# Kernel tuning notes

Measured on AMD Instinct MI355X. Metric: run time of the kernel, lower is better.

## Reference

```python
import jax, jax.numpy as jnp
import numpy as np

H, B, N, F, O = 8, 2, 2048, 256, 64
NEG_INF = jnp.float32(-9e15)


def _xavier(key, shape):
    fan_in, fan_out = shape[-2], shape[-1]
    limit = np.sqrt(6.0 / (fan_in + fan_out))
    return jax.random.uniform(key, shape, dtype=jnp.float32, minval=-limit, maxval=limit)


def setup_inputs() -> dict:
    key = jax.random.key(0)
    k1, k2, k3, k4, k5 = jax.random.split(key, 5)
    x = jax.random.normal(k1, (B, N, F), dtype=jnp.float32)
    adj = (jax.random.uniform(k2, (B, N, N)) < 0.05).astype(jnp.float32)
    adj = jnp.maximum(adj, jnp.eye(N, dtype=jnp.float32))
    W = _xavier(k3, (H, F, O))           # self.linear
    a_src = _xavier(k4, (H, O, 1))       # attention_vect_src
    a_dst = _xavier(k5, (H, O, 1))       # attention_vect_dst
    return {"x": x, "adj": adj, "W": W, "a_src": a_src, "a_dst": a_dst}


def reference(x, adj, W, a_src, a_dst):
    # h: [H, B, N, O]  (per-head linear projection)
    h = jnp.einsum('bnf,hfo->hbno', x, W)
    # additive attention scalars per node: [H, B, N]
    s_src = jnp.einsum('hbno,ho->hbn', h, a_src[..., 0])
    s_dst = jnp.einsum('hbno,ho->hbn', h, a_dst[..., 0])
    # score[h,b,i,j] = s_dst[i] + s_src[j]  -> [H, B, N, N]
    score = s_dst[..., :, None] + s_src[..., None, :]
    score = jax.nn.leaky_relu(score, negative_slope=0.2)
    score = jnp.where(adj > 0, score, NEG_INF)
    att = jax.nn.softmax(score, axis=-1) * adj  # dropout = identity (eval)
    # weighted aggregation of neighbor features: [H, B, N, O]
    out = jnp.einsum('hbij,hbjo->hbio', att, h)
    # concat heads along feature dim (head order preserved): [B, N, H*O]
    out = jnp.transpose(out, (1, 2, 0, 3)).reshape(B, N, H * O)
    return jax.nn.relu(out)
```

## Files before the change

### kernel.cpp

```cpp
#include <hip/hip_runtime.h>

#define H_ 8
#define B_ 2
#define N_ 2048
#define F_ 256
#define O_ 64
#define CAP 256

typedef unsigned short u16;
typedef unsigned int   u32;
typedef __attribute__((ext_vector_type(8))) short bf16x8;
typedef __attribute__((ext_vector_type(4))) float f32x4;

__device__ __forceinline__ float us2f(u16 u) {
    union { u32 i; float f; } c; c.i = ((u32)u) << 16; return c.f;
}
__device__ __forceinline__ float hi2f(u32 w) {
    union { u32 i; float f; } c; c.i = w & 0xFFFF0000u; return c.f;
}
__device__ __forceinline__ float lo2f(u32 w) {
    union { u32 i; float f; } c; c.i = w << 16; return c.f;
}
__device__ __forceinline__ u16 f2us_rn(float f) {
    union { float f; u32 i; } c; c.f = f;
    u32 r = c.i + 0x7FFFu + ((c.i >> 16) & 1u);
    return (u16)(r >> 16);
}
__device__ __forceinline__ int detect_bf(const void* adj) {
    u32 w0 = *(const u32*)adj;
    return (w0 & 0xFFFFu) == 0x3F80u;
}

__global__ __launch_bounds__(256) void wt_kernel(const void* __restrict__ W,
                                                 const void* __restrict__ adj,
                                                 u16* __restrict__ Wt) {
    int bf = detect_bf(adj);
    int g  = blockIdx.x * 256 + threadIdx.x;
    int h  = g >> 11;
    int o  = (g >> 5) & 63;
    int fc = g & 31;
    u16 tmp[8];
    if (bf) {
        const u16* wg = (const u16*)W + (size_t)h * F_ * O_ + o;
#pragma unroll
        for (int q = 0; q < 8; ++q) tmp[q] = wg[(size_t)(fc * 8 + q) * O_];
    } else {
        const float* wg = (const float*)W + (size_t)h * F_ * O_ + o;
#pragma unroll
        for (int q = 0; q < 8; ++q) tmp[q] = f2us_rn(wg[(size_t)(fc * 8 + q) * O_]);
    }
    *(uint4*)(Wt + (size_t)h * O_ * F_ + (size_t)o * F_ + fc * 8) = *(uint4*)tmp;
}

__global__ __launch_bounds__(256) void proj_kernel(const void* __restrict__ x,
                                                   const u16* __restrict__ Wt,
                                                   const void* __restrict__ a_src,
                                                   const void* __restrict__ a_dst,
                                                   const void* __restrict__ adj,
                                                   u16* __restrict__ hTb,
                                                   float* __restrict__ sTsrc,
                                                   float* __restrict__ sTdst) {
    int bf   = detect_bf(adj);
    int bx   = blockIdx.x;
    int h    = bx & 7;
    int bn0  = (bx >> 3) * 64;
    int tid  = threadIdx.x;
    int wave = tid >> 6;
    int lane = tid & 63;
    int m_l  = lane & 15;
    int quad = lane >> 4;
    int mrow = bn0 + wave * 16 + m_l;

    const u16* wtb = Wt + (size_t)h * O_ * F_;

    f32x4 acc[4] = {{0,0,0,0},{0,0,0,0},{0,0,0,0},{0,0,0,0}};
#pragma unroll
    for (int ks = 0; ks < 8; ++ks) {
        int kofs = ks * 32 + quad * 8;
        bf16x8 afrag;
        if (bf) {
            afrag = *(const bf16x8*)((const u16*)x + (size_t)mrow * F_ + kofs);
        } else {
            const float* xr = (const float*)x + (size_t)mrow * F_ + kofs;
#pragma unroll
            for (int q = 0; q < 8; ++q) afrag[q] = (short)f2us_rn(xr[q]);
        }
#pragma unroll
        for (int nt = 0; nt < 4; ++nt) {
            bf16x8 bfrag = *(const bf16x8*)(wtb + (size_t)(nt * 16 + m_l) * F_ + kofs);
            acc[nt] = __builtin_amdgcn_mfma_f32_16x16x32_bf16(afrag, bfrag, acc[nt], 0, 0, 0);
        }
    }

    float asv[4], adv[4];
#pragma unroll
    for (int nt = 0; nt < 4; ++nt) {
        int o = nt * 16 + m_l;
        if (bf) {
            asv[nt] = us2f(((const u16*)a_src)[h * 64 + o]);
            adv[nt] = us2f(((const u16*)a_dst)[h * 64 + o]);
        } else {
            asv[nt] = ((const float*)a_src)[h * 64 + o];
            adv[nt] = ((const float*)a_dst)[h * 64 + o];
        }
    }
    float vs[4] = {0,0,0,0}, vd[4] = {0,0,0,0};
#pragma unroll
    for (int nt = 0; nt < 4; ++nt)
#pragma unroll
        for (int r = 0; r < 4; ++r) {
            float hv = acc[nt][r];
            int row = wave * 16 + quad * 4 + r;
            hTb[(size_t)(bn0 + row) * 512 + h * 64 + nt * 16 + m_l] = f2us_rn(hv);
            vs[r] = fmaf(hv, asv[nt], vs[r]);
            vd[r] = fmaf(hv, adv[nt], vd[r]);
        }
#pragma unroll
    for (int r = 0; r < 4; ++r)
#pragma unroll
        for (int off = 1; off < 16; off <<= 1) {
            vs[r] += __shfl_xor(vs[r], off);
            vd[r] += __shfl_xor(vd[r], off);
        }
    if (m_l == 0) {
#pragma unroll
        for (int r = 0; r < 4; ++r) {
            int row = wave * 16 + quad * 4 + r;
            sTsrc[(size_t)(bn0 + row) * H_ + h] = vs[r];
            sTdst[(size_t)(bn0 + row) * H_ + h] = vd[r];
        }
    }
}

__global__ __launch_bounds__(256) void GATLayer_88072599371930_kernel(
        const u16* __restrict__ hTb,
        const float* __restrict__ sTsrc,
        const float* __restrict__ sTdst,
        const void* __restrict__ adj,
        float* __restrict__ out) {
    __shared__ int   scnt;
    __shared__ u16   sj[CAP];
    __shared__ float se[CAP * H_];
    __shared__ float mh[H_];
    __shared__ float rzh[H_];
    __shared__ float sdl[H_];
    __shared__ float sred[8 * 192];

    int bi   = blockIdx.x;
    int tid  = threadIdx.x;
    int base = bi & ~(N_ - 1);
    int bf   = detect_bf(adj);

    if (tid == 0) scnt = 0;
    if (tid < 8) sdl[tid] = sTdst[(size_t)bi * H_ + tid];
    __syncthreads();

    if (bf) {
        const u16* arow = (const u16*)adj + (size_t)bi * N_;
        uint4 v = *(const uint4*)(arow + tid * 8);
        u32 w[4] = {v.x, v.y, v.z, v.w};
        int j0 = tid * 8;
#pragma unroll
        for (int q = 0; q < 4; ++q) {
            if (w[q] & 0xFFFFu) { int p = atomicAdd(&scnt, 1); if (p < CAP) sj[p] = (u16)(j0 + 2 * q); }
            if (w[q] >> 16)     { int p = atomicAdd(&scnt, 1); if (p < CAP) sj[p] = (u16)(j0 + 2 * q + 1); }
        }
    } else {
        const float* arow = (const float*)adj + (size_t)bi * N_;
        for (int j = tid; j < N_; j += 256) {
            if (arow[j] > 0.f) { int p = atomicAdd(&scnt, 1); if (p < CAP) sj[p] = (u16)j; }
        }
    }
    __syncthreads();
    int n = scnt < CAP ? scnt : CAP;

    if (n <= 0) {
        out[(size_t)bi * 512 + tid] = 999.0f;
        out[(size_t)bi * 512 + 256 + tid] = 999.0f;
        return;
    }

    int tot = n * H_;
    for (int idx = tid; idx < tot; idx += 256) {
        int k  = idx >> 3;
        int hh = idx & 7;
        int j  = sj[k];
        float v = sdl[hh] + sTsrc[(size_t)(base + j) * H_ + hh];
        v = v > 0.f ? v : 0.2f * v;
        se[idx] = v;
    }
    __syncthreads();

    if (tid < 64) {
        int hh = tid >> 3, kk = tid & 7;
        float lm = -3.4e38f;
        for (int k = kk; k < n; k += 8) lm = fmaxf(lm, se[k * 8 + hh]);
#pragma unroll
        for (int mm = 1; mm < 8; mm <<= 1) lm = fmaxf(lm, __shfl_xor(lm, mm));
        if (kk == 0) mh[hh] = lm;
    }
    __syncthreads();
    for (int idx = tid; idx < tot; idx += 256) {
        int hh = idx & 7;
        se[idx] = __expf(se[idx] - mh[hh]);
    }
    __syncthreads();
    if (tid < 64) {
        int hh = tid >> 3, kk = tid & 7;
        float ls = 0.f;
        for (int k = kk; k < n; k += 8) ls += se[k * 8 + hh];
#pragma unroll
        for (int mm = 1; mm < 8; mm <<= 1) ls += __shfl_xor(ls, mm);
        if (kk == 0) rzh[hh] = 1.f / ls;
    }
    __syncthreads();

    int wv   = tid >> 6;
    int lane = tid & 63;
    int hh   = lane >> 3;
    int oq8  = lane & 7;
    const u16* hb = hTb + (size_t)base * 512 + hh * 64 + oq8 * 8;

    float a0 = 0.f, a1 = 0.f, a2 = 0.f, a3 = 0.f;
    float a4 = 0.f, a5 = 0.f, a6 = 0.f, a7 = 0.f;
    int k = wv;
    for (; k + 4 < n; k += 8) {
        int   j0 = sj[k], j1 = sj[k + 4];
        float w0 = se[k * 8 + hh], w1 = se[(k + 4) * 8 + hh];
        uint4 v0 = *(const uint4*)(hb + (size_t)j0 * 512);
        uint4 v1 = *(const uint4*)(hb + (size_t)j1 * 512);
        a0 = fmaf(w0, lo2f(v0.x), a0); a1 = fmaf(w0, hi2f(v0.x), a1);
        a2 = fmaf(w0, lo2f(v0.y), a2); a3 = fmaf(w0, hi2f(v0.y), a3);
        a4 = fmaf(w0, lo2f(v0.z), a4); a5 = fmaf(w0, hi2f(v0.z), a5);
        a6 = fmaf(w0, lo2f(v0.w), a6); a7 = fmaf(w0, hi2f(v0.w), a7);
        a0 = fmaf(w1, lo2f(v1.x), a0); a1 = fmaf(w1, hi2f(v1.x), a1);
        a2 = fmaf(w1, lo2f(v1.y), a2); a3 = fmaf(w1, hi2f(v1.y), a3);
        a4 = fmaf(w1, lo2f(v1.z), a4); a5 = fmaf(w1, hi2f(v1.z), a5);
        a6 = fmaf(w1, lo2f(v1.w), a6); a7 = fmaf(w1, hi2f(v1.w), a7);
    }
    for (; k < n; k += 4) {
        int   j = sj[k];
        float w = se[k * 8 + hh];
        uint4 v = *(const uint4*)(hb + (size_t)j * 512);
        a0 = fmaf(w, lo2f(v.x), a0); a1 = fmaf(w, hi2f(v.x), a1);
        a2 = fmaf(w, lo2f(v.y), a2); a3 = fmaf(w, hi2f(v.y), a3);
        a4 = fmaf(w, lo2f(v.z), a4); a5 = fmaf(w, hi2f(v.z), a5);
        a6 = fmaf(w, lo2f(v.w), a6); a7 = fmaf(w, hi2f(v.w), a7);
    }

    if (wv) {
        int p = (wv - 1) * 64 + lane;
        sred[0 * 192 + p] = a0; sred[1 * 192 + p] = a1;
        sred[2 * 192 + p] = a2; sred[3 * 192 + p] = a3;
        sred[4 * 192 + p] = a4; sred[5 * 192 + p] = a5;
        sred[6 * 192 + p] = a6; sred[7 * 192 + p] = a7;
    }
    __syncthreads();
    if (wv == 0) {
        float r[8] = {a0, a1, a2, a3, a4, a5, a6, a7};
        float rz = rzh[hh];
#pragma unroll
        for (int e = 0; e < 8; ++e) {
            float t = r[e] + sred[e * 192 + lane] + sred[e * 192 + 64 + lane]
                           + sred[e * 192 + 128 + lane];
            r[e] = fmaxf(t * rz, 0.f);
        }
        float4 o0; o0.x = r[0]; o0.y = r[1]; o0.z = r[2]; o0.w = r[3];
        float4 o1; o1.x = r[4]; o1.y = r[5]; o1.z = r[6]; o1.w = r[7];
        float* op = out + (size_t)bi * 512 + hh * 64 + oq8 * 8;
        *(float4*)op = o0;
        *(float4*)(op + 4) = o1;
    }
}

extern "C" void kernel_launch(void* const* d_in, const int* in_sizes, int n_in,
                              void* d_out, int out_size, void* d_ws, size_t ws_size,
                              hipStream_t stream) {
    const void *x = 0, *adj = 0, *W = 0, *a_src = 0, *a_dst = 0;
    for (int i = 0; i < n_in; ++i) {
        long sz = in_sizes[i];
        if (sz == (long)B_ * N_ * F_)      x = d_in[i];
        else if (sz == (long)B_ * N_ * N_) adj = d_in[i];
        else if (sz == (long)H_ * F_ * O_) W = d_in[i];
        else if (sz == (long)H_ * O_) { if (!a_src) a_src = d_in[i]; else a_dst = d_in[i]; }
    }
    if (!x)     x     = d_in[0];
    if (!adj)   adj   = d_in[1];
    if (!W)     W     = d_in[2];
    if (!a_src) a_src = d_in[3];
    if (!a_dst) a_dst = d_in[4];

    float* out = (float*)d_out;

    char* ws = (char*)d_ws;
    size_t off = 0;
    u16*   hTb   = (u16*)(ws + off);   off += (size_t)B_ * N_ * H_ * O_ * 2;
    float* sTsrc = (float*)(ws + off); off += (size_t)B_ * N_ * H_ * 4;
    float* sTdst = (float*)(ws + off); off += (size_t)B_ * N_ * H_ * 4;
    u16*   Wt    = (u16*)(ws + off);   off += (size_t)H_ * O_ * F_ * 2;

    wt_kernel<<<dim3(64), dim3(256), 0, stream>>>(W, adj, Wt);
    proj_kernel<<<dim3((N_ * B_ / 64) * H_), dim3(256), 0, stream>>>(
        x, Wt, a_src, a_dst, adj, hTb, sTsrc, sTdst);
    GATLayer_88072599371930_kernel<<<dim3(B_ * N_), dim3(256), 0, stream>>>(
        hTb, sTsrc, sTdst, adj, out);
}
```

Before: 128.5 us.

## Replace sparse gather aggregation with dense bitmask-masked MFMA attention tiles

The per-row sparse gather (atomic neighbor compaction, softmax over compacted list, scalar FMA aggregation) becomes a dense flash-style scheme. A prep kernel packs the adjacency into bitmasks and also does the W transpose. The main kernel processes 16 rows by 2 heads per block, computing masked exp scores into LDS as bf16 and multiplying them against a transposed h layout with MFMA. The softmax max is replaced by an upper bound (leaky_relu of s_dst plus the global max of s_src), which avoids a separate max pass but does dense O(N^2) work on a ~5% sparse matrix and risks underflow or precision loss in the bf16 probabilities.

```diff
diff --git a/kernel.cpp b/kernel.cpp
--- a/kernel.cpp
+++ b/kernel.cpp
@@ -5,7 +5,7 @@
 #define N_ 2048
 #define F_ 256
 #define O_ 64
-#define CAP 256
+#define PPAD 264
 
 typedef unsigned short u16;
 typedef unsigned int   u32;
@@ -15,12 +15,6 @@
 __device__ __forceinline__ float us2f(u16 u) {
     union { u32 i; float f; } c; c.i = ((u32)u) << 16; return c.f;
 }
-__device__ __forceinline__ float hi2f(u32 w) {
-    union { u32 i; float f; } c; c.i = w & 0xFFFF0000u; return c.f;
-}
-__device__ __forceinline__ float lo2f(u32 w) {
-    union { u32 i; float f; } c; c.i = w << 16; return c.f;
-}
 __device__ __forceinline__ u16 f2us_rn(float f) {
     union { float f; u32 i; } c; c.f = f;
     u32 r = c.i + 0x7FFFu + ((c.i >> 16) & 1u);
@@ -31,25 +25,55 @@
     return (w0 & 0xFFFFu) == 0x3F80u;
 }
 
-__global__ __launch_bounds__(256) void wt_kernel(const void* __restrict__ W,
-                                                 const void* __restrict__ adj,
-                                                 u16* __restrict__ Wt) {
-    int bf = detect_bf(adj);
-    int g  = blockIdx.x * 256 + threadIdx.x;
-    int h  = g >> 11;
-    int o  = (g >> 5) & 63;
-    int fc = g & 31;
-    u16 tmp[8];
-    if (bf) {
-        const u16* wg = (const u16*)W + (size_t)h * F_ * O_ + o;
-#pragma unroll
-        for (int q = 0; q < 8; ++q) tmp[q] = wg[(size_t)(fc * 8 + q) * O_];
+__global__ __launch_bounds__(256) void prep_kernel(const void* __restrict__ adj,
+                                                   const void* __restrict__ W,
+                                                   u32* __restrict__ mbg,
+                                                   u16* __restrict__ Wt) {
+    int blk = blockIdx.x;
+    int t   = threadIdx.x;
+    int bf  = detect_bf(adj);
+    if (blk < B_ * N_) {
+        __shared__ unsigned char bytes[256];
+        unsigned m8 = 0;
+        if (bf) {
+            const u16* arow = (const u16*)adj + (size_t)blk * N_;
+            uint4 v = *(const uint4*)(arow + t * 8);
+            u32 w[4] = {v.x, v.y, v.z, v.w};
+#pragma unroll
+            for (int q = 0; q < 4; ++q) {
+                if (w[q] & 0xFFFFu) m8 |= 1u << (2 * q);
+                if (w[q] >> 16)     m8 |= 1u << (2 * q + 1);
+            }
+        } else {
+            const float* arow = (const float*)adj + (size_t)blk * N_;
+#pragma unroll
+            for (int q = 0; q < 8; ++q)
+                if (arow[t * 8 + q] > 0.f) m8 |= 1u << q;
+        }
+        bytes[t] = (unsigned char)m8;
+        __syncthreads();
+        if (t < 64) {
+            u32 w = (u32)bytes[4 * t] | ((u32)bytes[4 * t + 1] << 8)
+                  | ((u32)bytes[4 * t + 2] << 16) | ((u32)bytes[4 * t + 3] << 24);
+            mbg[(size_t)blk * 64 + t] = w;
+        }
     } else {
-        const float* wg = (const float*)W + (size_t)h * F_ * O_ + o;
-#pragma unroll
-        for (int q = 0; q < 8; ++q) tmp[q] = f2us_rn(wg[(size_t)(fc * 8 + q) * O_]);
-    }
-    *(uint4*)(Wt + (size_t)h * O_ * F_ + (size_t)o * F_ + fc * 8) = *(uint4*)tmp;
+        int g  = (blk - B_ * N_) * 256 + t;
+        int h  = g >> 11;
+        int o  = (g >> 5) & 63;
+        int fc = g & 31;
+        u16 tmp[8];
+        if (bf) {
+            const u16* wg = (const u16*)W + (size_t)h * F_ * O_ + o;
+#pragma unroll
+            for (int q = 0; q < 8; ++q) tmp[q] = wg[(size_t)(fc * 8 + q) * O_];
+        } else {
+            const float* wg = (const float*)W + (size_t)h * F_ * O_ + o;
+#pragma unroll
+            for (int q = 0; q < 8; ++q) tmp[q] = f2us_rn(wg[(size_t)(fc * 8 + q) * O_]);
+        }
+        *(uint4*)(Wt + (size_t)h * O_ * F_ + (size_t)o * F_ + fc * 8) = *(uint4*)tmp;
+    }
 }
 
 __global__ __launch_bounds__(256) void proj_kernel(const void* __restrict__ x,
@@ -57,9 +81,9 @@
                                                    const void* __restrict__ a_src,
                                                    const void* __restrict__ a_dst,
                                                    const void* __restrict__ adj,
-                                                   u16* __restrict__ hTb,
-                                                   float* __restrict__ sTsrc,
-                                                   float* __restrict__ sTdst) {
+                                                   u16* __restrict__ hTv,
+                                                   float* __restrict__ sTvs,
+                                                   float* __restrict__ sTvd) {
     int bf   = detect_bf(adj);
     int bx   = blockIdx.x;
     int h    = bx & 7;
@@ -106,15 +130,18 @@
     }
     float vs[4] = {0,0,0,0}, vd[4] = {0,0,0,0};
 #pragma unroll
-    for (int nt = 0; nt < 4; ++nt)
+    for (int nt = 0; nt < 4; ++nt) {
+        alignas(8) u16 pk[4];
 #pragma unroll
         for (int r = 0; r < 4; ++r) {
             float hv = acc[nt][r];
-            int row = wave * 16 + quad * 4 + r;
-            hTb[(size_t)(bn0 + row) * 512 + h * 64 + nt * 16 + m_l] = f2us_rn(hv);
+            pk[r] = f2us_rn(hv);
             vs[r] = fmaf(hv, asv[nt], vs[r]);
             vd[r] = fmaf(hv, adv[nt], vd[r]);
         }
+        *(uint2*)(hTv + ((size_t)h * 64 + nt * 16 + m_l) * (B_ * N_)
+                      + bn0 + wave * 16 + quad * 4) = *(uint2*)pk;
+    }
 #pragma unroll
     for (int r = 0; r < 4; ++r)
 #pragma unroll
@@ -125,152 +152,116 @@
     if (m_l == 0) {
 #pragma unroll
         for (int r = 0; r < 4; ++r) {
-            int row = wave * 16 + quad * 4 + r;
-            sTsrc[(size_t)(bn0 + row) * H_ + h] = vs[r];
-            sTdst[(size_t)(bn0 + row) * H_ + h] = vd[r];
+            int row = bn0 + wave * 16 + quad * 4 + r;
+            sTvs[(size_t)h * (B_ * N_) + row] = vs[r];
+            sTvd[(size_t)h * (B_ * N_) + row] = vd[r];
         }
     }
 }
 
 __global__ __launch_bounds__(256) void GATLayer_88072599371930_kernel(
-        const u16* __restrict__ hTb,
-        const float* __restrict__ sTsrc,
-        const float* __restrict__ sTdst,
-        const void* __restrict__ adj,
+        const u16* __restrict__ hTv,
+        const float* __restrict__ sTvs,
+        const float* __restrict__ sTvd,
+        const u32* __restrict__ mbg,
         float* __restrict__ out) {
-    __shared__ int   scnt;
-    __shared__ u16   sj[CAP];
-    __shared__ float se[CAP * H_];
-    __shared__ float mh[H_];
-    __shared__ float rzh[H_];
-    __shared__ float sdl[H_];
-    __shared__ float sred[8 * 192];
-
-    int bi   = blockIdx.x;
-    int tid  = threadIdx.x;
-    int base = bi & ~(N_ - 1);
-    int bf   = detect_bf(adj);
-
-    if (tid == 0) scnt = 0;
-    if (tid < 8) sdl[tid] = sTdst[(size_t)bi * H_ + tid];
+    __shared__ u32   mask[16 * 64];
+    __shared__ u16   Pl[16 * PPAD];
+    __shared__ float ssl[2 * 256];
+    __shared__ float sdl[32], Mi[32], Zl[32], Mxs[2], wred[8];
+
+    int blk = blockIdx.x;
+    int hp  = blk & 3;
+    int itg = blk >> 2;
+    int b   = itg >> 7;
+    int i0  = (itg & 127) * 16;
+    int bbase = b * N_;
+    int h0  = hp * 2;
+    int tid = threadIdx.x, wv = tid >> 6, lane = tid & 63;
+    int m_l = lane & 15, quad = lane >> 4;
+
+    ((uint4*)mask)[tid] = *((const uint4*)(mbg + (size_t)(bbase + i0) * 64) + tid);
+    if (tid < 32) {
+        int i = tid >> 1, hh = tid & 1;
+        sdl[tid] = sTvd[(size_t)(h0 + hh) * (B_ * N_) + bbase + i0 + i];
+        Zl[tid]  = 0.f;
+    }
+    float mx0 = -3.4e38f, mx1 = -3.4e38f;
+    for (int n = tid; n < N_; n += 256) {
+        mx0 = fmaxf(mx0, sTvs[(size_t)h0 * (B_ * N_) + bbase + n]);
+        mx1 = fmaxf(mx1, sTvs[(size_t)(h0 + 1) * (B_ * N_) + bbase + n]);
+    }
+#pragma unroll
+    for (int off = 32; off; off >>= 1) {
+        mx0 = fmaxf(mx0, __shfl_xor(mx0, off));
+        mx1 = fmaxf(mx1, __shfl_xor(mx1, off));
+    }
+    if (lane == 0) { wred[wv] = mx0; wred[4 + wv] = mx1; }
     __syncthreads();
-
-    if (bf) {
-        const u16* arow = (const u16*)adj + (size_t)bi * N_;
-        uint4 v = *(const uint4*)(arow + tid * 8);
-        u32 w[4] = {v.x, v.y, v.z, v.w};
-        int j0 = tid * 8;
-#pragma unroll
-        for (int q = 0; q < 4; ++q) {
-            if (w[q] & 0xFFFFu) { int p = atomicAdd(&scnt, 1); if (p < CAP) sj[p] = (u16)(j0 + 2 * q); }
-            if (w[q] >> 16)     { int p = atomicAdd(&scnt, 1); if (p < CAP) sj[p] = (u16)(j0 + 2 * q + 1); }
-        }
-    } else {
-        const float* arow = (const float*)adj + (size_t)bi * N_;
-        for (int j = tid; j < N_; j += 256) {
-            if (arow[j] > 0.f) { int p = atomicAdd(&scnt, 1); if (p < CAP) sj[p] = (u16)j; }
-        }
-    }
+    if (tid == 0) Mxs[0] = fmaxf(fmaxf(wred[0], wred[1]), fmaxf(wred[2], wred[3]));
+    if (tid == 1) Mxs[1] = fmaxf(fmaxf(wred[4], wred[5]), fmaxf(wred[6], wred[7]));
     __syncthreads();
-    int n = scnt < CAP ? scnt : CAP;
-
-    if (n <= 0) {
-        out[(size_t)bi * 512 + tid] = 999.0f;
-        out[(size_t)bi * 512 + 256 + tid] = 999.0f;
-        return;
-    }
-
-    int tot = n * H_;
-    for (int idx = tid; idx < tot; idx += 256) {
-        int k  = idx >> 3;
-        int hh = idx & 7;
-        int j  = sj[k];
-        float v = sdl[hh] + sTsrc[(size_t)(base + j) * H_ + hh];
-        v = v > 0.f ? v : 0.2f * v;
-        se[idx] = v;
-    }
-    __syncthreads();
-
-    if (tid < 64) {
-        int hh = tid >> 3, kk = tid & 7;
-        float lm = -3.4e38f;
-        for (int k = kk; k < n; k += 8) lm = fmaxf(lm, se[k * 8 + hh]);
-#pragma unroll
-        for (int mm = 1; mm < 8; mm <<= 1) lm = fmaxf(lm, __shfl_xor(lm, mm));
-        if (kk == 0) mh[hh] = lm;
-    }
-    __syncthreads();
-    for (int idx = tid; idx < tot; idx += 256) {
-        int hh = idx & 7;
-        se[idx] = __expf(se[idx] - mh[hh]);
-    }
-    __syncthreads();
-    if (tid < 64) {
-        int hh = tid >> 3, kk = tid & 7;
-        float ls = 0.f;
-        for (int k = kk; k < n; k += 8) ls += se[k * 8 + hh];
-#pragma unroll
-        for (int mm = 1; mm < 8; mm <<= 1) ls += __shfl_xor(ls, mm);
-        if (kk == 0) rzh[hh] = 1.f / ls;
-    }
-    __syncthreads();
-
-    int wv   = tid >> 6;
-    int lane = tid & 63;
-    int hh   = lane >> 3;
-    int oq8  = lane & 7;
-    const u16* hb = hTb + (size_t)base * 512 + hh * 64 + oq8 * 8;
-
-    float a0 = 0.f, a1 = 0.f, a2 = 0.f, a3 = 0.f;
-    float a4 = 0.f, a5 = 0.f, a6 = 0.f, a7 = 0.f;
-    int k = wv;
-    for (; k + 4 < n; k += 8) {
-        int   j0 = sj[k], j1 = sj[k + 4];
-        float w0 = se[k * 8 + hh], w1 = se[(k + 4) * 8 + hh];
-        uint4 v0 = *(const uint4*)(hb + (size_t)j0 * 512);
-        uint4 v1 = *(const uint4*)(hb + (size_t)j1 * 512);
-        a0 = fmaf(w0, lo2f(v0.x), a0); a1 = fmaf(w0, hi2f(v0.x), a1);
-        a2 = fmaf(w0, lo2f(v0.y), a2); a3 = fmaf(w0, hi2f(v0.y), a3);
-        a4 = fmaf(w0, lo2f(v0.z), a4); a5 = fmaf(w0, hi2f(v0.z), a5);
-        a6 = fmaf(w0, lo2f(v0.w), a6); a7 = fmaf(w0, hi2f(v0.w), a7);
-        a0 = fmaf(w1, lo2f(v1.x), a0); a1 = fmaf(w1, hi2f(v1.x), a1);
-        a2 = fmaf(w1, lo2f(v1.y), a2); a3 = fmaf(w1, hi2f(v1.y), a3);
-        a4 = fmaf(w1, lo2f(v1.z), a4); a5 = fmaf(w1, hi2f(v1.z), a5);
-        a6 = fmaf(w1, lo2f(v1.w), a6); a7 = fmaf(w1, hi2f(v1.w), a7);
-    }
-    for (; k < n; k += 4) {
-        int   j = sj[k];
-        float w = se[k * 8 + hh];
-        uint4 v = *(const uint4*)(hb + (size_t)j * 512);
-        a0 = fmaf(w, lo2f(v.x), a0); a1 = fmaf(w, hi2f(v.x), a1);
-        a2 = fmaf(w, lo2f(v.y), a2); a3 = fmaf(w, hi2f(v.y), a3);
-        a4 = fmaf(w, lo2f(v.z), a4); a5 = fmaf(w, hi2f(v.z), a5);
-        a6 = fmaf(w, lo2f(v.w), a6); a7 = fmaf(w, hi2f(v.w), a7);
-    }
-
-    if (wv) {
-        int p = (wv - 1) * 64 + lane;
-        sred[0 * 192 + p] = a0; sred[1 * 192 + p] = a1;
-        sred[2 * 192 + p] = a2; sred[3 * 192 + p] = a3;
-        sred[4 * 192 + p] = a4; sred[5 * 192 + p] = a5;
-        sred[6 * 192 + p] = a6; sred[7 * 192 + p] = a7;
-    }
-    __syncthreads();
-    if (wv == 0) {
-        float r[8] = {a0, a1, a2, a3, a4, a5, a6, a7};
-        float rz = rzh[hh];
-#pragma unroll
-        for (int e = 0; e < 8; ++e) {
-            float t = r[e] + sred[e * 192 + lane] + sred[e * 192 + 64 + lane]
-                           + sred[e * 192 + 128 + lane];
-            r[e] = fmaxf(t * rz, 0.f);
-        }
-        float4 o0; o0.x = r[0]; o0.y = r[1]; o0.z = r[2]; o0.w = r[3];
-        float4 o1; o1.x = r[4]; o1.y = r[5]; o1.z = r[6]; o1.w = r[7];
-        float* op = out + (size_t)bi * 512 + hh * 64 + oq8 * 8;
-        *(float4*)op = o0;
-        *(float4*)(op + 4) = o1;
-    }
+    if (tid < 32) {
+        int hh = tid & 1;
+        float v = sdl[tid] + Mxs[hh];
+        Mi[tid] = v > 0.f ? v : 0.2f * v;
+    }
+
+    f32x4 acc[2] = {{0,0,0,0},{0,0,0,0}};
+    int pi = tid & 15, js = tid >> 4;
+
+    for (int jt = 0; jt < 8; ++jt) {
+        __syncthreads();
+        ssl[tid]       = sTvs[(size_t)h0 * (B_ * N_) + bbase + jt * 256 + tid];
+        ssl[256 + tid] = sTvs[(size_t)(h0 + 1) * (B_ * N_) + bbase + jt * 256 + tid];
+        __syncthreads();
+#pragma unroll
+        for (int hh = 0; hh < 2; ++hh) {
+            if (hh) __syncthreads();
+            {
+                u32 word = mask[pi * 64 + jt * 8 + (js >> 1)];
+                u32 bits = (word >> ((js & 1) * 16)) & 0xFFFFu;
+                float sdv = sdl[pi * 2 + hh];
+                float miv = Mi[pi * 2 + hh];
+                float zs = 0.f;
+                alignas(16) u16 pv[16];
+#pragma unroll
+                for (int q = 0; q < 16; ++q) {
+                    float ss = ssl[hh * 256 + js * 16 + q];
+                    float v = sdv + ss;
+                    v = v > 0.f ? v : 0.2f * v;
+                    float e = ((bits >> q) & 1u) ? __expf(v - miv) : 0.f;
+                    zs += e;
+                    pv[q] = f2us_rn(e);
+                }
+                *(uint4*)(Pl + pi * PPAD + js * 16)     = *(uint4*)(pv);
+                *(uint4*)(Pl + pi * PPAD + js * 16 + 8) = *(uint4*)(pv + 8);
+                atomicAdd(&Zl[pi * 2 + hh], zs);
+            }
+            __syncthreads();
+            {
+                const u16* bp = hTv + ((size_t)(h0 + hh) * 64 + wv * 16 + m_l) * (B_ * N_)
+                                    + bbase + jt * 256 + quad * 8;
+#pragma unroll
+                for (int ks = 0; ks < 8; ++ks) {
+                    bf16x8 af  = *(const bf16x8*)(Pl + m_l * PPAD + ks * 32 + quad * 8);
+                    bf16x8 bfr = *(const bf16x8*)(bp + ks * 32);
+                    acc[hh] = __builtin_amdgcn_mfma_f32_16x16x32_bf16(af, bfr, acc[hh], 0, 0, 0);
+                }
+            }
+        }
+    }
+
+#pragma unroll
+    for (int hh = 0; hh < 2; ++hh)
+#pragma unroll
+        for (int r = 0; r < 4; ++r) {
+            int ii = quad * 4 + r;
+            float z  = Zl[ii * 2 + hh];
+            float rz = z > 0.f ? 1.f / z : 0.f;
+            float v  = fmaxf(acc[hh][r] * rz, 0.f);
+            out[(size_t)(bbase + i0 + ii) * 512 + (h0 + hh) * 64 + wv * 16 + m_l] = v;
+        }
 }
 
 extern "C" void kernel_launch(void* const* d_in, const int* in_sizes, int n_in,
@@ -294,14 +285,15 @@
 
     char* ws = (char*)d_ws;
     size_t off = 0;
-    u16*   hTb   = (u16*)(ws + off);   off += (size_t)B_ * N_ * H_ * O_ * 2;
-    float* sTsrc = (float*)(ws + off); off += (size_t)B_ * N_ * H_ * 4;
-    float* sTdst = (float*)(ws + off); off += (size_t)B_ * N_ * H_ * 4;
-    u16*   Wt    = (u16*)(ws + off);   off += (size_t)H_ * O_ * F_ * 2;
-
-    wt_kernel<<<dim3(64), dim3(256), 0, stream>>>(W, adj, Wt);
+    u16*   hTv  = (u16*)(ws + off);   off += (size_t)H_ * O_ * B_ * N_ * 2;
+    float* sTvs = (float*)(ws + off); off += (size_t)H_ * B_ * N_ * 4;
+    float* sTvd = (float*)(ws + off); off += (size_t)H_ * B_ * N_ * 4;
+    u16*   Wt   = (u16*)(ws + off);   off += (size_t)H_ * O_ * F_ * 2;
+    u32*   mbg  = (u32*)(ws + off);   off += (size_t)B_ * N_ * 64 * 4;
+
+    prep_kernel<<<dim3(B_ * N_ + 64), dim3(256), 0, stream>>>(adj, W, mbg, Wt);
     proj_kernel<<<dim3((N_ * B_ / 64) * H_), dim3(256), 0, stream>>>(
-        x, Wt, a_src, a_dst, adj, hTb, sTsrc, sTdst);
-    GATLayer_88072599371930_kernel<<<dim3(B_ * N_), dim3(256), 0, stream>>>(
-        hTb, sTsrc, sTdst, adj, out);
-}
+        x, Wt, a_src, a_dst, adj, hTv, sTvs, sTvd);
+    GATLayer_88072599371930_kernel<<<dim3(B_ * N_ / 16 * 4), dim3(256), 0, stream>>>(
+        hTv, sTvs, sTvd, mbg, out);
+}
```

Result: slower. 175.4 us (+36.5%).

## Move adjacency compaction into prep kernel and fuse per-head softmax passes

Applied to the files above, without the earlier changes.

Adjacency row compaction moves out of the attention kernel into a prep kernel that also transposes W. The prep kernel uses a prefix scan instead of shared atomics, so neighbor order is now deterministic. The attention kernel reads precomputed neighbor lists and head-major score arrays. Each wave handles two heads' softmax with wave-level reductions instead of four block-wide passes, uses a padded stride-9 score layout, and unrolls the gather loop 4x. The cost is an extra global round trip for neighbor indices and a separate full pass over the adjacency before the projection.

```diff
diff --git a/kernel.cpp b/kernel.cpp
--- a/kernel.cpp
+++ b/kernel.cpp
@@ -6,6 +6,7 @@
 #define F_ 256
 #define O_ 64
 #define CAP 256
+#define SE9(k, h) ((k) * 9 + (h))
 
 typedef unsigned short u16;
 typedef unsigned int   u32;
@@ -31,25 +32,75 @@
     return (w0 & 0xFFFFu) == 0x3F80u;
 }
 
-__global__ __launch_bounds__(256) void wt_kernel(const void* __restrict__ W,
-                                                 const void* __restrict__ adj,
-                                                 u16* __restrict__ Wt) {
-    int bf = detect_bf(adj);
-    int g  = blockIdx.x * 256 + threadIdx.x;
-    int h  = g >> 11;
-    int o  = (g >> 5) & 63;
-    int fc = g & 31;
-    u16 tmp[8];
-    if (bf) {
-        const u16* wg = (const u16*)W + (size_t)h * F_ * O_ + o;
-#pragma unroll
-        for (int q = 0; q < 8; ++q) tmp[q] = wg[(size_t)(fc * 8 + q) * O_];
+__global__ __launch_bounds__(256) void prep_kernel(const void* __restrict__ adj,
+                                                   const void* __restrict__ W,
+                                                   int* __restrict__ cnt,
+                                                   u16* __restrict__ nidx,
+                                                   u16* __restrict__ Wt) {
+    int blk = blockIdx.x;
+    int t   = threadIdx.x;
+    int bf  = detect_bf(adj);
+    if (blk < B_ * N_) {
+        __shared__ u16 sidx[CAP];
+        __shared__ int scan[256];
+        unsigned m8 = 0;
+        if (bf) {
+            const u16* arow = (const u16*)adj + (size_t)blk * N_;
+            uint4 v = *(const uint4*)(arow + t * 8);
+            u32 w[4] = {v.x, v.y, v.z, v.w};
+#pragma unroll
+            for (int q = 0; q < 4; ++q) {
+                if (w[q] & 0xFFFFu) m8 |= 1u << (2 * q);
+                if (w[q] >> 16)     m8 |= 1u << (2 * q + 1);
+            }
+        } else {
+            const float* arow = (const float*)adj + (size_t)blk * N_;
+#pragma unroll
+            for (int q = 0; q < 8; ++q)
+                if (arow[t * 8 + q] > 0.f) m8 |= 1u << q;
+        }
+        int c = __popc(m8);
+        scan[t] = c;
+        __syncthreads();
+#pragma unroll
+        for (int d = 1; d < 256; d <<= 1) {
+            int v = (t >= d) ? scan[t - d] : 0;
+            __syncthreads();
+            scan[t] += v;
+            __syncthreads();
+        }
+        int ofs = scan[t] - c;
+        int total = scan[255];
+        int j0 = t * 8;
+        int p  = ofs;
+#pragma unroll
+        for (int q = 0; q < 8; ++q) {
+            if ((m8 >> q) & 1u) {
+                if (p < CAP) sidx[p] = (u16)(j0 + q);
+                ++p;
+            }
+        }
+        __syncthreads();
+        int m = total < CAP ? total : CAP;
+        if (t == 0) cnt[blk] = m;
+        for (int k = t; k < m; k += 256) nidx[(size_t)blk * CAP + k] = sidx[k];
     } else {
-        const float* wg = (const float*)W + (size_t)h * F_ * O_ + o;
-#pragma unroll
-        for (int q = 0; q < 8; ++q) tmp[q] = f2us_rn(wg[(size_t)(fc * 8 + q) * O_]);
-    }
-    *(uint4*)(Wt + (size_t)h * O_ * F_ + (size_t)o * F_ + fc * 8) = *(uint4*)tmp;
+        int g  = (blk - B_ * N_) * 256 + t;
+        int h  = g >> 11;
+        int o  = (g >> 5) & 63;
+        int fc = g & 31;
+        u16 tmp[8];
+        if (bf) {
+            const u16* wg = (const u16*)W + (size_t)h * F_ * O_ + o;
+#pragma unroll
+            for (int q = 0; q < 8; ++q) tmp[q] = wg[(size_t)(fc * 8 + q) * O_];
+        } else {
+            const float* wg = (const float*)W + (size_t)h * F_ * O_ + o;
+#pragma unroll
+            for (int q = 0; q < 8; ++q) tmp[q] = f2us_rn(wg[(size_t)(fc * 8 + q) * O_]);
+        }
+        *(uint4*)(Wt + (size_t)h * O_ * F_ + (size_t)o * F_ + fc * 8) = *(uint4*)tmp;
+    }
 }
 
 __global__ __launch_bounds__(256) void proj_kernel(const void* __restrict__ x,
@@ -58,8 +109,8 @@
                                                    const void* __restrict__ a_dst,
                                                    const void* __restrict__ adj,
                                                    u16* __restrict__ hTb,
-                                                   float* __restrict__ sTsrc,
-                                                   float* __restrict__ sTdst) {
+                                                   float* __restrict__ sTvs,
+                                                   float* __restrict__ sTvd) {
     int bf   = detect_bf(adj);
     int bx   = blockIdx.x;
     int h    = bx & 7;
@@ -110,8 +161,8 @@
 #pragma unroll
         for (int r = 0; r < 4; ++r) {
             float hv = acc[nt][r];
-            int row = wave * 16 + quad * 4 + r;
-            hTb[(size_t)(bn0 + row) * 512 + h * 64 + nt * 16 + m_l] = f2us_rn(hv);
+            hTb[(size_t)(bn0 + wave * 16 + quad * 4 + r) * 512 + h * 64 + nt * 16 + m_l]
+                = f2us_rn(hv);
             vs[r] = fmaf(hv, asv[nt], vs[r]);
             vd[r] = fmaf(hv, adv[nt], vd[r]);
         }
@@ -125,23 +176,22 @@
     if (m_l == 0) {
 #pragma unroll
         for (int r = 0; r < 4; ++r) {
-            int row = wave * 16 + quad * 4 + r;
-            sTsrc[(size_t)(bn0 + row) * H_ + h] = vs[r];
-            sTdst[(size_t)(bn0 + row) * H_ + h] = vd[r];
+            int row = bn0 + wave * 16 + quad * 4 + r;
+            sTvs[(size_t)h * (B_ * N_) + row] = vs[r];
+            sTvd[(size_t)h * (B_ * N_) + row] = vd[r];
         }
     }
 }
 
 __global__ __launch_bounds__(256) void GATLayer_88072599371930_kernel(
         const u16* __restrict__ hTb,
-        const float* __restrict__ sTsrc,
-        const float* __restrict__ sTdst,
-        const void* __restrict__ adj,
+        const float* __restrict__ sTvs,
+        const float* __restrict__ sTvd,
+        const int* __restrict__ cnt,
+        const u16* __restrict__ nidx,
         float* __restrict__ out) {
-    __shared__ int   scnt;
     __shared__ u16   sj[CAP];
-    __shared__ float se[CAP * H_];
-    __shared__ float mh[H_];
+    __shared__ float se[CAP * 9];
     __shared__ float rzh[H_];
     __shared__ float sdl[H_];
     __shared__ float sred[8 * 192];
@@ -149,86 +199,55 @@
     int bi   = blockIdx.x;
     int tid  = threadIdx.x;
     int base = bi & ~(N_ - 1);
-    int bf   = detect_bf(adj);
-
-    if (tid == 0) scnt = 0;
-    if (tid < 8) sdl[tid] = sTdst[(size_t)bi * H_ + tid];
-    __syncthreads();
-
-    if (bf) {
-        const u16* arow = (const u16*)adj + (size_t)bi * N_;
-        uint4 v = *(const uint4*)(arow + tid * 8);
-        u32 w[4] = {v.x, v.y, v.z, v.w};
-        int j0 = tid * 8;
-#pragma unroll
-        for (int q = 0; q < 4; ++q) {
-            if (w[q] & 0xFFFFu) { int p = atomicAdd(&scnt, 1); if (p < CAP) sj[p] = (u16)(j0 + 2 * q); }
-            if (w[q] >> 16)     { int p = atomicAdd(&scnt, 1); if (p < CAP) sj[p] = (u16)(j0 + 2 * q + 1); }
-        }
-    } else {
-        const float* arow = (const float*)adj + (size_t)bi * N_;
-        for (int j = tid; j < N_; j += 256) {
-            if (arow[j] > 0.f) { int p = atomicAdd(&scnt, 1); if (p < CAP) sj[p] = (u16)j; }
-        }
-    }
-    __syncthreads();
-    int n = scnt < CAP ? scnt : CAP;
-
-    if (n <= 0) {
-        out[(size_t)bi * 512 + tid] = 999.0f;
-        out[(size_t)bi * 512 + 256 + tid] = 999.0f;
-        return;
-    }
-
-    int tot = n * H_;
-    for (int idx = tid; idx < tot; idx += 256) {
-        int k  = idx >> 3;
-        int hh = idx & 7;
-        int j  = sj[k];
-        float v = sdl[hh] + sTsrc[(size_t)(base + j) * H_ + hh];
-        v = v > 0.f ? v : 0.2f * v;
-        se[idx] = v;
-    }
-    __syncthreads();
-
-    if (tid < 64) {
-        int hh = tid >> 3, kk = tid & 7;
-        float lm = -3.4e38f;
-        for (int k = kk; k < n; k += 8) lm = fmaxf(lm, se[k * 8 + hh]);
-#pragma unroll
-        for (int mm = 1; mm < 8; mm <<= 1) lm = fmaxf(lm, __shfl_xor(lm, mm));
-        if (kk == 0) mh[hh] = lm;
-    }
-    __syncthreads();
-    for (int idx = tid; idx < tot; idx += 256) {
-        int hh = idx & 7;
-        se[idx] = __expf(se[idx] - mh[hh]);
-    }
-    __syncthreads();
-    if (tid < 64) {
-        int hh = tid >> 3, kk = tid & 7;
-        float ls = 0.f;
-        for (int k = kk; k < n; k += 8) ls += se[k * 8 + hh];
-#pragma unroll
-        for (int mm = 1; mm < 8; mm <<= 1) ls += __shfl_xor(ls, mm);
-        if (kk == 0) rzh[hh] = 1.f / ls;
-    }
-    __syncthreads();
-
     int wv   = tid >> 6;
     int lane = tid & 63;
-    int hh   = lane >> 3;
-    int oq8  = lane & 7;
+
+    if (tid < 32) ((uint4*)sj)[tid] = ((const uint4*)(nidx + (size_t)bi * CAP))[tid];
+    if (tid < 8)  sdl[tid] = sTvd[(size_t)tid * (B_ * N_) + bi];
+    int n = cnt[bi];
+    __syncthreads();
+
+#pragma unroll
+    for (int hi = 0; hi < 2; ++hi) {
+        int hh = wv * 2 + hi;
+        float sd = sdl[hh];
+        const float* ssb = sTvs + (size_t)hh * (B_ * N_) + base;
+        float lm = -3.4e38f;
+        for (int k = lane; k < n; k += 64) {
+            float v = sd + ssb[sj[k]];
+            v = v > 0.f ? v : 0.2f * v;
+            se[SE9(k, hh)] = v;
+            lm = fmaxf(lm, v);
+        }
+#pragma unroll
+        for (int off = 32; off; off >>= 1) lm = fmaxf(lm, __shfl_xor(lm, off));
+        float ls = 0.f;
+        for (int k = lane; k < n; k += 64) {
+            float e = __expf(se[SE9(k, hh)] - lm);
+            se[SE9(k, hh)] = e;
+            ls += e;
+        }
+#pragma unroll
+        for (int off = 32; off; off >>= 1) ls += __shfl_xor(ls, off);
+        if (lane == 0) rzh[hh] = 1.f / ls;
+    }
+    __syncthreads();
+
+    int hh  = lane >> 3;
+    int oq8 = lane & 7;
     const u16* hb = hTb + (size_t)base * 512 + hh * 64 + oq8 * 8;
 
     float a0 = 0.f, a1 = 0.f, a2 = 0.f, a3 = 0.f;
     float a4 = 0.f, a5 = 0.f, a6 = 0.f, a7 = 0.f;
     int k = wv;
-    for (; k + 4 < n; k += 8) {
-        int   j0 = sj[k], j1 = sj[k + 4];
-        float w0 = se[k * 8 + hh], w1 = se[(k + 4) * 8 + hh];
+    for (; k + 12 < n; k += 16) {
+        int   j0 = sj[k],     j1 = sj[k + 4],  j2 = sj[k + 8],  j3 = sj[k + 12];
+        float w0 = se[SE9(k, hh)],      w1 = se[SE9(k + 4, hh)];
+        float w2 = se[SE9(k + 8, hh)],  w3 = se[SE9(k + 12, hh)];
         uint4 v0 = *(const uint4*)(hb + (size_t)j0 * 512);
         uint4 v1 = *(const uint4*)(hb + (size_t)j1 * 512);
+        uint4 v2 = *(const uint4*)(hb + (size_t)j2 * 512);
+        uint4 v3 = *(const uint4*)(hb + (size_t)j3 * 512);
         a0 = fmaf(w0, lo2f(v0.x), a0); a1 = fmaf(w0, hi2f(v0.x), a1);
         a2 = fmaf(w0, lo2f(v0.y), a2); a3 = fmaf(w0, hi2f(v0.y), a3);
         a4 = fmaf(w0, lo2f(v0.z), a4); a5 = fmaf(w0, hi2f(v0.z), a5);
@@ -237,10 +256,18 @@
         a2 = fmaf(w1, lo2f(v1.y), a2); a3 = fmaf(w1, hi2f(v1.y), a3);
         a4 = fmaf(w1, lo2f(v1.z), a4); a5 = fmaf(w1, hi2f(v1.z), a5);
         a6 = fmaf(w1, lo2f(v1.w), a6); a7 = fmaf(w1, hi2f(v1.w), a7);
+        a0 = fmaf(w2, lo2f(v2.x), a0); a1 = fmaf(w2, hi2f(v2.x), a1);
+        a2 = fmaf(w2, lo2f(v2.y), a2); a3 = fmaf(w2, hi2f(v2.y), a3);
+        a4 = fmaf(w2, lo2f(v2.z), a4); a5 = fmaf(w2, hi2f(v2.z), a5);
+        a6 = fmaf(w2, lo2f(v2.w), a6); a7 = fmaf(w2, hi2f(v2.w), a7);
+        a0 = fmaf(w3, lo2f(v3.x), a0); a1 = fmaf(w3, hi2f(v3.x), a1);
+        a2 = fmaf(w3, lo2f(v3.y), a2); a3 = fmaf(w3, hi2f(v3.y), a3);
+        a4 = fmaf(w3, lo2f(v3.z), a4); a5 = fmaf(w3, hi2f(v3.z), a5);
+        a6 = fmaf(w3, lo2f(v3.w), a6); a7 = fmaf(w3, hi2f(v3.w), a7);
     }
     for (; k < n; k += 4) {
         int   j = sj[k];
-        float w = se[k * 8 + hh];
+        float w = se[SE9(k, hh)];
         uint4 v = *(const uint4*)(hb + (size_t)j * 512);
         a0 = fmaf(w, lo2f(v.x), a0); a1 = fmaf(w, hi2f(v.x), a1);
         a2 = fmaf(w, lo2f(v.y), a2); a3 = fmaf(w, hi2f(v.y), a3);
@@ -294,14 +321,16 @@
 
     char* ws = (char*)d_ws;
     size_t off = 0;
-    u16*   hTb   = (u16*)(ws + off);   off += (size_t)B_ * N_ * H_ * O_ * 2;
-    float* sTsrc = (float*)(ws + off); off += (size_t)B_ * N_ * H_ * 4;
-    float* sTdst = (float*)(ws + off); off += (size_t)B_ * N_ * H_ * 4;
-    u16*   Wt    = (u16*)(ws + off);   off += (size_t)H_ * O_ * F_ * 2;
-
-    wt_kernel<<<dim3(64), dim3(256), 0, stream>>>(W, adj, Wt);
+    u16*   hTb  = (u16*)(ws + off);   off += (size_t)B_ * N_ * H_ * O_ * 2;
+    float* sTvs = (float*)(ws + off); off += (size_t)H_ * B_ * N_ * 4;
+    float* sTvd = (float*)(ws + off); off += (size_t)H_ * B_ * N_ * 4;
+    u16*   Wt   = (u16*)(ws + off);   off += (size_t)H_ * O_ * F_ * 2;
+    int*   cnt  = (int*)(ws + off);   off += (size_t)B_ * N_ * 4;
+    u16*   nidx = (u16*)(ws + off);   off += (size_t)B_ * N_ * CAP * 2;
+
+    prep_kernel<<<dim3(B_ * N_ + 64), dim3(256), 0, stream>>>(adj, W, cnt, nidx, Wt);
     proj_kernel<<<dim3((N_ * B_ / 64) * H_), dim3(256), 0, stream>>>(
-        x, Wt, a_src, a_dst, adj, hTb, sTsrc, sTdst);
+        x, Wt, a_src, a_dst, adj, hTb, sTvs, sTvd);
     GATLayer_88072599371930_kernel<<<dim3(B_ * N_), dim3(256), 0, stream>>>(
-        hTb, sTsrc, sTdst, adj, out);
-}
+        hTb, sTvs, sTvd, cnt, nidx, out);
+}
```

Result: no change. 127.3 us (median of 2 runs) (-0.9%).
